# Kernel optimization log

Measured on AMD Instinct MI355X. Metric: run time of the kernel, lower is better.

Reference implementation:

```python
import jax, jax.numpy as jnp
import numpy as np

N = 100000   # nodes
E = 1600000  # edges
G = 512      # graphs in batch
IN_C, H1, H2, OUT_C = 3, 64, 128, 2


def setup_inputs() -> dict:
    key = jax.random.key(0)
    ks = jax.random.split(key, 9)
    x = jax.random.normal(ks[0], (N, IN_C), dtype=jnp.float32)
    edge_index = jax.random.randint(ks[1], (2, E), 0, N, dtype=jnp.int64)
    batch = jnp.sort(jax.random.randint(ks[2], (N,), 0, G, dtype=jnp.int64))
    # Glorot-ish init for weights, zeros for biases (as PyG GCNConv / nn.Linear defaults roughly)
    def glorot(k, shape):
        lim = float(np.sqrt(6.0 / (shape[0] + shape[1])))
        return jax.random.uniform(k, shape, jnp.float32, -lim, lim)
    W1 = glorot(ks[3], (IN_C, H1)); b1 = jnp.zeros((H1,), jnp.float32)
    W2 = glorot(ks[4], (H1, H2));   b2 = jnp.zeros((H2,), jnp.float32)
    Wfc = glorot(ks[5], (H2, OUT_C)); bfc = jnp.zeros((OUT_C,), jnp.float32)
    return {"x": x, "edge_index": edge_index, "batch": batch,
            "W1": W1, "b1": b1, "W2": W2, "b2": b2, "Wfc": Wfc, "bfc": bfc}


def _gcn_conv(x, W, b, src, dst, dinv):
    # PyG GCNConv: out = D^{-1/2} (A + I) D^{-1/2} X W + b
    xw = x @ W                                    # [N, F]
    norm = dinv[src] * dinv[dst]                  # per-edge symmetric norm
    agg = jax.ops.segment_sum(norm[:, None] * xw[src], dst, num_segments=x.shape[0])
    agg = agg + (dinv * dinv)[:, None] * xw       # self-loop contribution
    return agg + b


def reference(x, edge_index, batch, W1, b1, W2, b2, Wfc, bfc):
    src, dst = edge_index[0], edge_index[1]
    # degree with self-loops (edge weight 1), counted at edge targets as in PyG
    deg = jax.ops.segment_sum(jnp.ones((E,), x.dtype), dst, num_segments=N) + 1.0
    dinv = jax.lax.rsqrt(deg)
    h = jax.nn.relu(_gcn_conv(x, W1, b1, src, dst, dinv))
    h = jax.nn.relu(_gcn_conv(h, W2, b2, src, dst, dinv))
    # global_mean_pool over batch indices
    sums = jax.ops.segment_sum(h, batch, num_segments=G)          # [G, H2]
    cnt = jax.ops.segment_sum(jnp.ones((N,), h.dtype), batch, num_segments=G)
    pooled = sums / jnp.maximum(cnt, 1.0)[:, None]
    return pooled @ Wfc + bfc
```

## Files before the change

kernel.cpp:

```cpp
#include <hip/hip_runtime.h>

#define NN 100000
#define NE 1600000
#define NG 512
#define C_H1 64
#define C_H2 128
#define C_OUT 2

#define MM2_BLOCKS ((NN + 127) / 128)
#define NB ((NN + 255) >> 8)
#define PCHUNKS 512
#define PCHUNK_E (NE / PCHUNKS)

__global__ void k_hist(const int* __restrict__ ei, int* __restrict__ hist) {
    __shared__ int lh[NB];
    int tid = threadIdx.x;
    int blk = blockIdx.x;
    for (int i = tid; i < NB; i += 256) lh[i] = 0;
    __syncthreads();
    int base = blk * PCHUNK_E;
    for (int e = base + tid; e < base + PCHUNK_E; e += 256)
        atomicAdd(&lh[ei[NE + e] >> 8], 1);
    __syncthreads();
    for (int i = tid; i < NB; i += 256) hist[i * PCHUNKS + blk] = lh[i];
}

__global__ void k_colscan0(const int* __restrict__ hist, int* __restrict__ offs,
                           int* __restrict__ btot) {
    __shared__ int sh[256];
    int b = blockIdx.x;
    int tid = threadIdx.x;
    int v0 = hist[b * PCHUNKS + 2 * tid];
    int v1 = hist[b * PCHUNKS + 2 * tid + 1];
    sh[tid] = v0 + v1;
    __syncthreads();
    for (int off = 1; off < 256; off <<= 1) {
        int v = (tid >= off) ? sh[tid - off] : 0;
        __syncthreads();
        sh[tid] += v;
        __syncthreads();
    }
    int base = (tid == 0) ? 0 : sh[tid - 1];
    offs[b * PCHUNKS + 2 * tid]     = base;
    offs[b * PCHUNKS + 2 * tid + 1] = base + v0;
    if (tid == 255) btot[b] = sh[255];
}

__global__ void k_bbase(const int* __restrict__ btot, int* __restrict__ bbase,
                        int* __restrict__ row_ptr) {
    __shared__ int sh[256];
    int tid = threadIdx.x;
    int v0 = (2 * tid     < NB) ? btot[2 * tid]     : 0;
    int v1 = (2 * tid + 1 < NB) ? btot[2 * tid + 1] : 0;
    sh[tid] = v0 + v1;
    __syncthreads();
    for (int off = 1; off < 256; off <<= 1) {
        int v = (tid >= off) ? sh[tid - off] : 0;
        __syncthreads();
        sh[tid] += v;
        __syncthreads();
    }
    int base = (tid == 0) ? 0 : sh[tid - 1];
    if (2 * tid     < NB) bbase[2 * tid]     = base;
    if (2 * tid + 1 < NB) bbase[2 * tid + 1] = base + v0;
    if (tid == 255) { bbase[NB] = sh[255]; row_ptr[NN] = sh[255]; }
}

__global__ void k_scatterA(const int* __restrict__ ei, const int* __restrict__ offs,
                           const int* __restrict__ bbase, int2* __restrict__ ed2) {
    __shared__ int lcur[NB];
    int tid = threadIdx.x;
    int blk = blockIdx.x;
    for (int i = tid; i < NB; i += 256) lcur[i] = bbase[i] + offs[i * PCHUNKS + blk];
    __syncthreads();
    int base = blk * PCHUNK_E;
    for (int e = base + tid; e < base + PCHUNK_E; e += 256) {
        int s = ei[e], d = ei[NE + e];
        int pos = atomicAdd(&lcur[d >> 8], 1);
        int2 v; v.x = s; v.y = d;
        ed2[pos] = v;
    }
}

__global__ void k_B1(const int2* __restrict__ ed2, const int* __restrict__ bbase,
                     float* __restrict__ dinv, int* __restrict__ row_ptr) {
    __shared__ int ldeg[256];
    __shared__ int sh[256];
    int b = blockIdx.x;
    int tid = threadIdx.x;
    int lo = b << 8;
    ldeg[tid] = 0;
    __syncthreads();
    int beg = bbase[b], end = bbase[b + 1];
    for (int j = beg + tid; j < end; j += 256)
        atomicAdd(&ldeg[ed2[j].y - lo], 1);
    __syncthreads();
    int d = ldeg[tid];
    int node = lo + tid;
    if (node < NN) dinv[node] = rsqrtf((float)d + 1.0f);
    sh[tid] = d;
    __syncthreads();
    for (int off = 1; off < 256; off <<= 1) {
        int v = (tid >= off) ? sh[tid - off] : 0;
        __syncthreads();
        sh[tid] += v;
        __syncthreads();
    }
    int excl = beg + ((tid == 0) ? 0 : sh[tid - 1]);
    if (node < NN) row_ptr[node] = excl;
}

__global__ void k_x4(const float* __restrict__ x, float4* __restrict__ x4) {
    int n = blockIdx.x * blockDim.x + threadIdx.x;
    if (n >= NN) return;
    float4 v; v.x = x[n * 3]; v.y = x[n * 3 + 1]; v.z = x[n * 3 + 2]; v.w = 0.f;
    x4[n] = v;
}

__global__ void k_scatterB(const int* __restrict__ row_ptr, const int2* __restrict__ ed2,
                           const float* __restrict__ dinv, const float4* __restrict__ x4,
                           int2* __restrict__ ed, float4* __restrict__ aggx4) {
    __shared__ int   lcur[256];
    __shared__ float ldin[256];
    __shared__ float lax[256 * 3];
    int b = blockIdx.x;
    int lo = b << 8;
    int tid = threadIdx.x;
    int node = lo + tid;
    if (node <= NN) lcur[tid] = row_ptr[node < NN ? node : NN];
    else            lcur[tid] = 0;
    ldin[tid] = (node < NN) ? dinv[node] : 0.f;
    lax[tid] = 0.f; lax[256 + tid] = 0.f; lax[512 + tid] = 0.f;
    __syncthreads();
    int seg_beg = row_ptr[lo];
    int hi = lo + 256; if (hi > NN) hi = NN;
    int seg_end = row_ptr[hi];
    for (int j = seg_beg + tid; j < seg_end; j += 256) {
        int2 sd = ed2[j];
        int local = sd.y - lo;
        int pos = atomicAdd(&lcur[local], 1);
        float nrm = dinv[sd.x] * ldin[local];
        int2 v; v.x = sd.x; v.y = __float_as_int(nrm);
        ed[pos] = v;
        float4 xs = x4[sd.x];
        atomicAdd(&lax[local],       nrm * xs.x);
        atomicAdd(&lax[256 + local], nrm * xs.y);
        atomicAdd(&lax[512 + local], nrm * xs.z);
    }
    __syncthreads();
    if (node < NN) {
        float di = ldin[tid];
        float s2 = di * di;
        float4 xs = x4[node];
        float4 a;
        a.x = lax[tid]       + s2 * xs.x;
        a.y = lax[256 + tid] + s2 * xs.y;
        a.z = lax[512 + tid] + s2 * xs.z;
        a.w = 0.f;
        aggx4[node] = a;
    }
}

__global__ void k_edge1(const int* __restrict__ row_ptr, const int2* __restrict__ ed,
                        const float4* __restrict__ aggx4, const float* __restrict__ dinv,
                        const float* __restrict__ W1, const float* __restrict__ b1,
                        float* __restrict__ agg1) {
    __shared__ float4 lp[256];
    int t = blockIdx.x * 256 + threadIdx.x;
    int n = t >> 6, c = t & 63;
    int lane = threadIdx.x & 63;
    int wbase = threadIdx.x & 192;

    float w0 = W1[c], w1 = W1[64 + c], w2 = W1[128 + c], bb = b1[c];
    float4 an = aggx4[n];
    float di = dinv[n];
    float hself = fmaxf(fmaf(an.x, w0, fmaf(an.y, w1, fmaf(an.z, w2, bb))), 0.f);
    float acc = di * di * hself;

    int beg = row_ptr[n], end = row_ptr[n + 1];
    for (int base = beg; base < end; base += 64) {
        int m = end - base; if (m > 64) m = 64;
        if (lane < m) {
            int2 v = ed[base + lane];
            float4 ax = aggx4[v.x];
            float4 p; p.x = ax.x; p.y = ax.y; p.z = ax.z; p.w = __int_as_float(v.y);
            lp[wbase + lane] = p;
        }
        int e = 0;
        for (; e + 3 < m; e += 4) {
            float4 p0 = lp[wbase + e];
            float4 p1 = lp[wbase + e + 1];
            float4 p2 = lp[wbase + e + 2];
            float4 p3 = lp[wbase + e + 3];
            float h0  = fmaxf(fmaf(p0.x, w0, fmaf(p0.y, w1, fmaf(p0.z, w2, bb))), 0.f);
            float h1v = fmaxf(fmaf(p1.x, w0, fmaf(p1.y, w1, fmaf(p1.z, w2, bb))), 0.f);
            float h2v = fmaxf(fmaf(p2.x, w0, fmaf(p2.y, w1, fmaf(p2.z, w2, bb))), 0.f);
            float h3v = fmaxf(fmaf(p3.x, w0, fmaf(p3.y, w1, fmaf(p3.z, w2, bb))), 0.f);
            acc = fmaf(p0.w, h0, acc);
            acc = fmaf(p1.w, h1v, acc);
            acc = fmaf(p2.w, h2v, acc);
            acc = fmaf(p3.w, h3v, acc);
        }
        for (; e < m; ++e) {
            float4 p = lp[wbase + e];
            float h = fmaxf(fmaf(p.x, w0, fmaf(p.y, w1, fmaf(p.z, w2, bb))), 0.f);
            acc = fmaf(p.w, h, acc);
        }
    }
    agg1[t] = acc;
}

__global__ void k_mm2pool(const float* __restrict__ agg1, const float* __restrict__ W2,
                          const float* __restrict__ b2, const int* __restrict__ batch,
                          float* __restrict__ pooled) {
    __shared__ float wt[C_H1 * C_H2];
    __shared__ float at[64 * C_H1];
    int tid = threadIdx.x;
    {
        const float4* w4 = (const float4*)W2;
        float4* wl = (float4*)wt;
        for (int i = tid; i < (C_H1 * C_H2) / 4; i += 256) wl[i] = w4[i];
    }
    int tx = tid & 31;
    int my = tid >> 5;
    int c0 = tx * 4;
    int m0 = my * 8;
    float bias[4];
#pragma unroll
    for (int j = 0; j < 4; ++j) bias[j] = b2[c0 + j];

    for (int tile = 0; tile < 2; ++tile) {
        {
            const float4* a4 = (const float4*)(agg1 + ((size_t)blockIdx.x * 128 + tile * 64) * C_H1);
            float4* al = (float4*)at;
            for (int i = tid; i < (64 * C_H1) / 4; i += 256) al[i] = a4[i];
        }
        __syncthreads();

        float acc[8][4];
#pragma unroll
        for (int i = 0; i < 8; ++i)
#pragma unroll
            for (int j = 0; j < 4; ++j) acc[i][j] = 0.f;

        for (int k0 = 0; k0 < C_H1; k0 += 4) {
            float4 wf[4];
#pragma unroll
            for (int kk = 0; kk < 4; ++kk)
                wf[kk] = *(const float4*)&wt[(k0 + kk) * C_H2 + c0];
#pragma unroll
            for (int i = 0; i < 8; ++i) {
                float4 af = *(const float4*)&at[(m0 + i) * C_H1 + k0];
                acc[i][0] = fmaf(af.x, wf[0].x, acc[i][0]);
                acc[i][1] = fmaf(af.x, wf[0].y, acc[i][1]);
                acc[i][2] = fmaf(af.x, wf[0].z, acc[i][2]);
                acc[i][3] = fmaf(af.x, wf[0].w, acc[i][3]);
                acc[i][0] = fmaf(af.y, wf[1].x, acc[i][0]);
                acc[i][1] = fmaf(af.y, wf[1].y, acc[i][1]);
                acc[i][2] = fmaf(af.y, wf[1].z, acc[i][2]);
                acc[i][3] = fmaf(af.y, wf[1].w, acc[i][3]);
                acc[i][0] = fmaf(af.z, wf[2].x, acc[i][0]);
                acc[i][1] = fmaf(af.z, wf[2].y, acc[i][1]);
                acc[i][2] = fmaf(af.z, wf[2].z, acc[i][2]);
                acc[i][3] = fmaf(af.z, wf[2].w, acc[i][3]);
                acc[i][0] = fmaf(af.w, wf[3].x, acc[i][0]);
                acc[i][1] = fmaf(af.w, wf[3].y, acc[i][1]);
                acc[i][2] = fmaf(af.w, wf[3].z, acc[i][2]);
                acc[i][3] = fmaf(af.w, wf[3].w, acc[i][3]);
            }
        }

        int nbase = blockIdx.x * 128 + tile * 64 + m0;
        int gidx[8];
#pragma unroll
        for (int i = 0; i < 8; ++i)
            gidx[i] = (nbase + i < NN) ? batch[nbase + i] : -1;

#pragma unroll
        for (int j = 0; j < 4; ++j) {
            int run_g = -1;
            float rs = 0.f;
#pragma unroll
            for (int i = 0; i < 8; ++i) {
                if (gidx[i] < 0) break;
                float h = fmaxf(acc[i][j] + bias[j], 0.f);
                if (gidx[i] != run_g) {
                    if (run_g >= 0) atomicAdd(&pooled[(run_g << 7) + c0 + j], rs);
                    run_g = gidx[i]; rs = h;
                } else {
                    rs += h;
                }
            }
            if (run_g >= 0) atomicAdd(&pooled[(run_g << 7) + c0 + j], rs);
        }
        __syncthreads();
    }
}

__device__ __forceinline__ int lower_bound(const int* __restrict__ a, int n, int key) {
    int lo = 0, hi = n;
    while (lo < hi) { int mid = (lo + hi) >> 1; if (a[mid] < key) lo = mid + 1; else hi = mid; }
    return lo;
}

__global__ void k_fc(const float* __restrict__ pooled, const int* __restrict__ batch,
                     const float* __restrict__ Wfc, const float* __restrict__ bfc,
                     float* __restrict__ out) {
    int t = blockIdx.x * blockDim.x + threadIdx.x;
    if (t >= NG * C_OUT) return;
    int g = t >> 1, o = t & 1;
    int start = lower_bound(batch, NN, g);
    int end   = lower_bound(batch, NN, g + 1);
    float inv = 1.f / fmaxf((float)(end - start), 1.f);
    float s = bfc[o];
    for (int cc = 0; cc < C_H2; ++cc)
        s = fmaf(pooled[(g << 7) + cc] * inv, Wfc[cc * C_OUT + o], s);
    out[t] = s;
}

extern "C" void kernel_launch(void* const* d_in, const int* in_sizes, int n_in,
                              void* d_out, int out_size, void* d_ws, size_t ws_size,
                              hipStream_t stream) {
    const float* x     = (const float*)d_in[0];
    const int*   ei    = (const int*)d_in[1];
    const int*   batch = (const int*)d_in[2];
    const float* W1    = (const float*)d_in[3];
    const float* b1    = (const float*)d_in[4];
    const float* W2    = (const float*)d_in[5];
    const float* b2    = (const float*)d_in[6];
    const float* Wfc   = (const float*)d_in[7];
    const float* bfc   = (const float*)d_in[8];
    float* out = (float*)d_out;

    char* p = (char*)d_ws;
    auto alloc = [&](size_t bytes) { char* r = p; p += (bytes + 255) & ~size_t(255); return r; };
    float*  dinv    = (float*) alloc((size_t)NN * 4);
    int*    row_ptr = (int*)   alloc((size_t)(NN + 1) * 4);
    int*    btot    = (int*)   alloc((size_t)NB * 4);
    int*    bbase   = (int*)   alloc((size_t)(NB + 1) * 4);
    int*    hist    = (int*)   alloc((size_t)NB * PCHUNKS * 4);
    int*    offs    = (int*)   alloc((size_t)NB * PCHUNKS * 4);
    int2*   ed2     = (int2*)  alloc((size_t)NE * 8);
    int2*   ed      = (int2*)  alloc((size_t)NE * 8);
    float4* x4      = (float4*)alloc((size_t)NN * 16);
    float4* aggx4   = (float4*)alloc((size_t)NN * 16);
    float*  agg1    = (float*) alloc((size_t)(NN + 128) * C_H1 * 4);
    float*  pooled  = (float*) alloc((size_t)NG * C_H2 * 4);

    hipMemsetAsync(pooled, 0, (size_t)NG * C_H2 * 4, stream);
    k_hist    <<<PCHUNKS, 256, 0, stream>>>(ei, hist);
    k_colscan0<<<NB, 256, 0, stream>>>(hist, offs, btot);
    k_bbase   <<<1, 256, 0, stream>>>(btot, bbase, row_ptr);
    k_scatterA<<<PCHUNKS, 256, 0, stream>>>(ei, offs, bbase, ed2);
    k_B1      <<<NB, 256, 0, stream>>>(ed2, bbase, dinv, row_ptr);
    k_x4      <<<(NN + 255) / 256, 256, 0, stream>>>(x, x4);
    k_scatterB<<<NB, 256, 0, stream>>>(row_ptr, ed2, dinv, x4, ed, aggx4);
    k_edge1   <<<(NN * C_H1) / 256, 256, 0, stream>>>(row_ptr, ed, aggx4, dinv, W1, b1, agg1);
    k_mm2pool <<<MM2_BLOCKS, 256, 0, stream>>>(agg1, W2, b2, batch, pooled);
    k_fc      <<<(NG * C_OUT + 255) / 256, 256, 0, stream>>>(pooled, batch, Wfc, bfc, out);
}
```

Measured before the change: 241.9 us.

## Compute full 128-row tile per block with 8x8 register tiles and LDS pool pre-reduction

The matmul-plus-pool kernel now loads all 128 rows of agg1 into padded shared memory (stride 68) at once instead of two 64-row tiles. Each thread computes an 8x8 output tile, which raises FMA-to-load reuse and removes a sync round. Per-graph partial sums for the first four graphs in the block are accumulated with shared-memory atomics and then flushed, cutting global atomic traffic. The costs are higher register pressure from 64 accumulators and more LDS use, both of which can lower occupancy.

```diff
diff --git a/kernel.cpp b/kernel.cpp
--- a/kernel.cpp
+++ b/kernel.cpp
@@ -11,6 +11,7 @@
 #define NB ((NN + 255) >> 8)
 #define PCHUNKS 512
 #define PCHUNK_E (NE / PCHUNKS)
+#define AT_S 68
 
 __global__ void k_hist(const int* __restrict__ ei, int* __restrict__ hist) {
     __shared__ int lh[NB];
@@ -214,86 +215,99 @@
                           const float* __restrict__ b2, const int* __restrict__ batch,
                           float* __restrict__ pooled) {
     __shared__ float wt[C_H1 * C_H2];
-    __shared__ float at[64 * C_H1];
+    __shared__ float at[128 * AT_S];
+    __shared__ float lpool[4 * C_H2];
     int tid = threadIdx.x;
     {
         const float4* w4 = (const float4*)W2;
         float4* wl = (float4*)wt;
         for (int i = tid; i < (C_H1 * C_H2) / 4; i += 256) wl[i] = w4[i];
-    }
-    int tx = tid & 31;
-    int my = tid >> 5;
-    int c0 = tx * 4;
+        const float4* a4 = (const float4*)(agg1 + (size_t)blockIdx.x * 128 * C_H1);
+        for (int i = tid; i < 128 * 16; i += 256) {
+            int row = i >> 4, k4 = i & 15;
+            *(float4*)&at[row * AT_S + k4 * 4] = a4[i];
+        }
+        for (int i = tid; i < 4 * C_H2; i += 256) lpool[i] = 0.f;
+    }
+    __syncthreads();
+
+    int tx = tid & 15;
+    int my = tid >> 4;
+    int c0 = tx * 8;
     int m0 = my * 8;
-    float bias[4];
-#pragma unroll
-    for (int j = 0; j < 4; ++j) bias[j] = b2[c0 + j];
-
-    for (int tile = 0; tile < 2; ++tile) {
-        {
-            const float4* a4 = (const float4*)(agg1 + ((size_t)blockIdx.x * 128 + tile * 64) * C_H1);
-            float4* al = (float4*)at;
-            for (int i = tid; i < (64 * C_H1) / 4; i += 256) al[i] = a4[i];
-        }
-        __syncthreads();
-
-        float acc[8][4];
-#pragma unroll
-        for (int i = 0; i < 8; ++i)
-#pragma unroll
-            for (int j = 0; j < 4; ++j) acc[i][j] = 0.f;
-
-        for (int k0 = 0; k0 < C_H1; k0 += 4) {
-            float4 wf[4];
-#pragma unroll
-            for (int kk = 0; kk < 4; ++kk)
-                wf[kk] = *(const float4*)&wt[(k0 + kk) * C_H2 + c0];
-#pragma unroll
-            for (int i = 0; i < 8; ++i) {
-                float4 af = *(const float4*)&at[(m0 + i) * C_H1 + k0];
-                acc[i][0] = fmaf(af.x, wf[0].x, acc[i][0]);
-                acc[i][1] = fmaf(af.x, wf[0].y, acc[i][1]);
-                acc[i][2] = fmaf(af.x, wf[0].z, acc[i][2]);
-                acc[i][3] = fmaf(af.x, wf[0].w, acc[i][3]);
-                acc[i][0] = fmaf(af.y, wf[1].x, acc[i][0]);
-                acc[i][1] = fmaf(af.y, wf[1].y, acc[i][1]);
-                acc[i][2] = fmaf(af.y, wf[1].z, acc[i][2]);
-                acc[i][3] = fmaf(af.y, wf[1].w, acc[i][3]);
-                acc[i][0] = fmaf(af.z, wf[2].x, acc[i][0]);
-                acc[i][1] = fmaf(af.z, wf[2].y, acc[i][1]);
-                acc[i][2] = fmaf(af.z, wf[2].z, acc[i][2]);
-                acc[i][3] = fmaf(af.z, wf[2].w, acc[i][3]);
-                acc[i][0] = fmaf(af.w, wf[3].x, acc[i][0]);
-                acc[i][1] = fmaf(af.w, wf[3].y, acc[i][1]);
-                acc[i][2] = fmaf(af.w, wf[3].z, acc[i][2]);
-                acc[i][3] = fmaf(af.w, wf[3].w, acc[i][3]);
+
+    float acc[8][8];
+#pragma unroll
+    for (int i = 0; i < 8; ++i)
+#pragma unroll
+        for (int j = 0; j < 8; ++j) acc[i][j] = 0.f;
+
+    for (int k0 = 0; k0 < C_H1; k0 += 4) {
+        float4 wf[4][2];
+#pragma unroll
+        for (int kk = 0; kk < 4; ++kk) {
+            wf[kk][0] = *(const float4*)&wt[(k0 + kk) * C_H2 + c0];
+            wf[kk][1] = *(const float4*)&wt[(k0 + kk) * C_H2 + c0 + 4];
+        }
+#pragma unroll
+        for (int i = 0; i < 8; ++i) {
+            float4 af = *(const float4*)&at[(m0 + i) * AT_S + k0];
+#pragma unroll
+            for (int kk = 0; kk < 4; ++kk) {
+                float a = (kk == 0) ? af.x : (kk == 1) ? af.y : (kk == 2) ? af.z : af.w;
+                acc[i][0] = fmaf(a, wf[kk][0].x, acc[i][0]);
+                acc[i][1] = fmaf(a, wf[kk][0].y, acc[i][1]);
+                acc[i][2] = fmaf(a, wf[kk][0].z, acc[i][2]);
+                acc[i][3] = fmaf(a, wf[kk][0].w, acc[i][3]);
+                acc[i][4] = fmaf(a, wf[kk][1].x, acc[i][4]);
+                acc[i][5] = fmaf(a, wf[kk][1].y, acc[i][5]);
+                acc[i][6] = fmaf(a, wf[kk][1].z, acc[i][6]);
+                acc[i][7] = fmaf(a, wf[kk][1].w, acc[i][7]);
             }
         }
-
-        int nbase = blockIdx.x * 128 + tile * 64 + m0;
-        int gidx[8];
-#pragma unroll
-        for (int i = 0; i < 8; ++i)
-            gidx[i] = (nbase + i < NN) ? batch[nbase + i] : -1;
-
-#pragma unroll
-        for (int j = 0; j < 4; ++j) {
-            int run_g = -1;
-            float rs = 0.f;
-#pragma unroll
-            for (int i = 0; i < 8; ++i) {
-                if (gidx[i] < 0) break;
-                float h = fmaxf(acc[i][j] + bias[j], 0.f);
-                if (gidx[i] != run_g) {
-                    if (run_g >= 0) atomicAdd(&pooled[(run_g << 7) + c0 + j], rs);
-                    run_g = gidx[i]; rs = h;
-                } else {
-                    rs += h;
+    }
+
+    int nbase = blockIdx.x * 128 + m0;
+    int gbase = batch[blockIdx.x * 128];
+    int gidx[8];
+#pragma unroll
+    for (int i = 0; i < 8; ++i)
+        gidx[i] = (nbase + i < NN) ? batch[nbase + i] : -1;
+    float bias[8];
+#pragma unroll
+    for (int j = 0; j < 8; ++j) bias[j] = b2[c0 + j];
+
+#pragma unroll
+    for (int j = 0; j < 8; ++j) {
+        int run_g = -1;
+        float rs = 0.f;
+#pragma unroll
+        for (int i = 0; i < 8; ++i) {
+            if (gidx[i] < 0) break;
+            float h = fmaxf(acc[i][j] + bias[j], 0.f);
+            if (gidx[i] != run_g) {
+                if (run_g >= 0) {
+                    int slot = run_g - gbase;
+                    if (slot < 4) atomicAdd(&lpool[slot * C_H2 + c0 + j], rs);
+                    else          atomicAdd(&pooled[(run_g << 7) + c0 + j], rs);
                 }
+                run_g = gidx[i]; rs = h;
+            } else {
+                rs += h;
             }
-            if (run_g >= 0) atomicAdd(&pooled[(run_g << 7) + c0 + j], rs);
-        }
-        __syncthreads();
+        }
+        if (run_g >= 0) {
+            int slot = run_g - gbase;
+            if (slot < 4) atomicAdd(&lpool[slot * C_H2 + c0 + j], rs);
+            else          atomicAdd(&pooled[(run_g << 7) + c0 + j], rs);
+        }
+    }
+    __syncthreads();
+    for (int i = tid; i < 4 * C_H2; i += 256) {
+        int slot = i >> 7, c = i & 127;
+        int g = gbase + slot;
+        float v = lpool[i];
+        if (g < NG && v != 0.f) atomicAdd(&pooled[(g << 7) + c], v);
     }
 }
 
```

New measurement: 231.1 us. 4.5% less time.
